# Optimization experiments

Measured on AMD Instinct MI355X. Metric: run time of the kernel, lower is better.

## Reference

```python
import jax, jax.numpy as jnp
import numpy as np

N_HEADS = 12
HIDDEN = 768  # NOTE: d_head == hidden_size in this module (unusual)

def setup_inputs() -> dict:
    key = jax.random.key(0)
    ks = jax.random.split(key, 4)
    b, s = 8, 512
    d3 = 3 * N_HEADS * HIDDEN
    return {
        "x": jax.random.normal(ks[0], (b, s, HIDDEN), dtype=jnp.float32),
        "mask": jnp.zeros((b, 1, 1, s), dtype=jnp.float32),
        "w_qkv": jax.random.normal(ks[1], (d3, HIDDEN), dtype=jnp.float32) * 0.02,
        "b_qkv": jnp.zeros((d3,), dtype=jnp.float32),
        "w_o": jax.random.normal(ks[2], (HIDDEN, N_HEADS * HIDDEN), dtype=jnp.float32) * 0.02,
        "b_o": jnp.zeros((HIDDEN,), dtype=jnp.float32),
    }

def reference(x, mask, w_qkv, b_qkv, w_o, b_o):
    b, s, _ = x.shape
    nh = N_HEADS * HIDDEN
    qkv = x @ w_qkv.T + b_qkv                      # (b, s, 3*n*h)
    q, k, v = jnp.split(qkv, 3, axis=-1)           # each (b, s, n*h)
    def heads(t):
        return t.reshape(b, s, N_HEADS, HIDDEN).transpose(0, 2, 1, 3)  # (b, n, s, h)
    q, k, v = heads(q), heads(k), heads(v)
    scale = 1.0 / np.sqrt(HIDDEN).astype(np.float32)
    scores = jnp.einsum('bnqh,bnkh->bnqk', q, k) * scale  # (b, n, s_q, s_k)
    scores = scores + mask                         # additive mask broadcast
    a = jax.nn.softmax(scores, axis=-1)
    av = jnp.einsum('bnqk,bnkh->bnqh', a, v)       # (b, n, s, h)
    h = av.transpose(0, 2, 1, 3).reshape(b, s, nh) # (b, s, n*h)
    return h @ w_o.T + b_o                         # (b, s, hidden)
```

## Files before the change

### kernel.cpp

```cpp
#include <hip/hip_runtime.h>
#include <hip/hip_bf16.h>
#include <stdint.h>

#define AS1 __attribute__((address_space(1)))
#define AS3 __attribute__((address_space(3)))

typedef __attribute__((ext_vector_type(8))) __bf16 bf16x8;
typedef __attribute__((ext_vector_type(4))) float f32x4;
typedef unsigned short u16;
typedef __attribute__((ext_vector_type(8))) unsigned short u16x8;

#define B_    8
#define S_    512
#define NH_   12
#define HD_   768
#define NHD_  (NH_*HD_)
#define D3_   (3*NHD_)
#define QKLD_ (2*NHD_)
#define QK_SCALE 0.03608439182435161f

__device__ __forceinline__ u16 f2bf(float x) {
  union { float f; unsigned u; } a; a.f = x;
  unsigned r = a.u + 0x7fffu + ((a.u >> 16) & 1u);
  return (u16)(r >> 16);
}
__device__ __forceinline__ float bf2f(u16 x) {
  union { unsigned u; float f; } a; a.u = ((unsigned)x) << 16; return a.f;
}

__device__ __forceinline__ void gload16(const void* g, void* l) {
  __builtin_amdgcn_global_load_lds((const AS1 void*)g, (AS3 void*)l, 16, 0, 0);
}

struct GP {
  const u16* A;
  const u16* B;
  int K, lda, ldb;
  long sAb, sAn, sBb, sBn;
  void* o0; void* o2;
  const float* bias;
};

template<int MODE>
__global__ __launch_bounds__(256)
void gemm_bt(GP p) {
  __shared__ __align__(16) char smem[32768];
  const int tid  = threadIdx.x;
  const int wave = tid >> 6, lane = tid & 63;
  const int wr = wave >> 1, wc = wave & 1;
  const int bm0 = blockIdx.y * 128;
  const int bn0 = blockIdx.x * 128;
  const int z   = blockIdx.z;
  const int zb  = z / NH_, zn = z - zb * NH_;

  const u16* A  = p.A + zb * p.sAb + zn * p.sAn;
  const u16* Bm = p.B + zb * p.sBb + zn * p.sBn;

  f32x4 acc[4][4];
  const f32x4 zero4 = {0.f, 0.f, 0.f, 0.f};
#pragma unroll
  for (int i = 0; i < 4; ++i)
#pragma unroll
    for (int j = 0; j < 4; ++j) acc[i][j] = zero4;

  const int scolsw = ((lane & 7) ^ (lane >> 3)) * 8;
  const u16* gA = A  + (size_t)(bm0 + wave*8 + (lane>>3)) * p.lda + scolsw;
  const u16* gB = Bm + (size_t)(bn0 + wave*8 + (lane>>3)) * p.ldb + scolsw;
  char* ldsA = smem;
  char* ldsB = smem + 16384;
  char* stA  = ldsA + wave*1024;
  char* stB  = ldsB + wave*1024;

  const int aRow = (wr*64 + (lane&15)) * 128;
  const int bRow = (wc*64 + (lane&15)) * 128;
  const int csw  = lane & 7;
  const int cOff0 = (((lane>>4)    ) ^ csw) << 4;
  const int cOff1 = ((4 + (lane>>4)) ^ csw) << 4;

  for (int k0 = 0; k0 < p.K; k0 += 64) {
#pragma unroll
    for (int i = 0; i < 4; ++i) {
      gload16(gA + (size_t)i*32*p.lda, stA + i*4096);
      gload16(gB + (size_t)i*32*p.ldb, stB + i*4096);
    }
    gA += 64; gB += 64;
    __syncthreads();
#pragma unroll
    for (int kk = 0; kk < 2; ++kk) {
      const int cOff = kk ? cOff1 : cOff0;
      bf16x8 av[4], bv[4];
#pragma unroll
      for (int i = 0; i < 4; ++i)
        av[i] = *(const bf16x8*)(ldsA + aRow + i*2048 + cOff);
#pragma unroll
      for (int j = 0; j < 4; ++j)
        bv[j] = *(const bf16x8*)(ldsB + bRow + j*2048 + cOff);
#pragma unroll
      for (int i = 0; i < 4; ++i)
#pragma unroll
        for (int j = 0; j < 4; ++j)
          acc[i][j] = __builtin_amdgcn_mfma_f32_16x16x32_bf16(av[i], bv[j], acc[i][j], 0, 0, 0);
    }
    __syncthreads();
  }

  const int r0 = bm0 + wr*64 + ((lane>>4) << 2);
  const int c0 = bn0 + wc*64 + (lane&15);

  if constexpr (MODE == 0) {
    if (bn0 < QKLD_) {
#pragma unroll
      for (int i = 0; i < 4; ++i) {
        u16* rbase = (u16*)p.o0 + (long)(r0 + i*16) * QKLD_;
#pragma unroll
        for (int j = 0; j < 4; ++j) {
          const int col = c0 + j*16;
          const float bs = p.bias[col];
#pragma unroll
          for (int r = 0; r < 4; ++r)
            rbase[(long)r * QKLD_ + col] = f2bf(acc[i][j][r] + bs);
        }
      }
    } else {
#pragma unroll
      for (int i = 0; i < 4; ++i) {
        const int rowq = r0 + i*16;
        const int s0 = rowq & 511;
        const int bb = rowq >> 9;
#pragma unroll
        for (int j = 0; j < 4; ++j) {
          const int col = c0 + j*16;
          const int vcol = col - QKLD_;
          const int n = vcol / HD_;
          const int h = vcol - n*HD_;
          const float bs = p.bias[col];
          ushort4 pk;
          pk.x = f2bf(acc[i][j][0] + bs);
          pk.y = f2bf(acc[i][j][1] + bs);
          pk.z = f2bf(acc[i][j][2] + bs);
          pk.w = f2bf(acc[i][j][3] + bs);
          *(ushort4*)((u16*)p.o2 + (long)(bb*NH_ + n)*(S_*HD_) + (long)h*S_ + s0) = pk;
        }
      }
    }
  } else {
#pragma unroll
    for (int i = 0; i < 4; ++i) {
#pragma unroll
      for (int j = 0; j < 4; ++j) {
        const int col = c0 + j*16;
#pragma unroll
        for (int r = 0; r < 4; ++r) {
          const int row = r0 + i*16 + r;
          const float v = acc[i][j][r];
          if constexpr (MODE == 1) {
            ((u16*)p.o0)[(long)z*S_*S_ + (long)row*S_ + col] = f2bf(v * QK_SCALE);
          } else if constexpr (MODE == 2) {
            ((u16*)p.o0)[(long)(zb*S_ + row)*QKLD_ + zn*HD_ + col] = f2bf(v);
          } else {
            ((float*)p.o0)[((long)z * gridDim.y * 128 + row) * HD_ + col] = v;
          }
        }
      }
    }
  }
}

__global__ __launch_bounds__(256)
void softmax_rows(u16* __restrict__ SP, const float* __restrict__ maskc) {
  const int wave = threadIdx.x >> 6, lane = threadIdx.x & 63;
  const int rid = blockIdx.x * 4 + wave;
  const int z = rid >> 9;
  const int b = z / NH_;
  const u16x8 sv = *(const u16x8*)(SP + (size_t)rid * S_ + lane*8);
  const float* mrow = maskc + (size_t)b * S_;
  float vals[8];
  float m = -3.4e38f;
#pragma unroll
  for (int j = 0; j < 8; ++j) {
    vals[j] = bf2f(sv[j]) + mrow[lane*8 + j];
    m = fmaxf(m, vals[j]);
  }
#pragma unroll
  for (int o = 32; o > 0; o >>= 1) m = fmaxf(m, __shfl_xor(m, o));
  float sum = 0.f;
#pragma unroll
  for (int j = 0; j < 8; ++j) { vals[j] = __expf(vals[j] - m); sum += vals[j]; }
#pragma unroll
  for (int o = 32; o > 0; o >>= 1) sum += __shfl_xor(sum, o);
  const float inv = 1.0f / sum;
  u16x8 pv;
#pragma unroll
  for (int j = 0; j < 8; ++j) pv[j] = f2bf(vals[j] * inv);
  *(u16x8*)(SP + (size_t)rid * S_ + lane*8) = pv;
}

__global__ __launch_bounds__(256)
void cvt_bf16(const float4* __restrict__ in, ushort4* __restrict__ out, int n4) {
  const int i = blockIdx.x * 256 + threadIdx.x;
  if (i >= n4) return;
  const float4 v = in[i];
  ushort4 o;
  o.x = f2bf(v.x); o.y = f2bf(v.y); o.z = f2bf(v.z); o.w = f2bf(v.w);
  out[i] = o;
}

__global__ __launch_bounds__(256)
void combine_out(const float4* __restrict__ part, const float* __restrict__ b,
                 float4* __restrict__ out, int n4) {
  const int i = blockIdx.x * 256 + threadIdx.x;
  if (i >= n4) return;
  const float4 a0 = part[i];
  const float4 a1 = part[i + (size_t)n4];
  const float4 a2 = part[i + (size_t)2*n4];
  const float4 a3 = part[i + (size_t)3*n4];
  const int c = (i * 4) % HD_;
  float4 o;
  o.x = a0.x + a1.x + a2.x + a3.x + b[c];
  o.y = a0.y + a1.y + a2.y + a3.y + b[c+1];
  o.z = a0.z + a1.z + a2.z + a3.z + b[c+2];
  o.w = a0.w + a1.w + a2.w + a3.w + b[c+3];
  out[i] = o;
}

extern "C" void kernel_launch(void* const* d_in, const int* in_sizes, int n_in,
                              void* d_out, int out_size, void* d_ws, size_t ws_size,
                              hipStream_t stream) {
  const float* x     = (const float*)d_in[0];
  const float* mask  = (const float*)d_in[1];
  const float* w_qkv = (const float*)d_in[2];
  const float* b_qkv = (const float*)d_in[3];
  const float* w_o   = (const float*)d_in[4];
  const float* b_o   = (const float*)d_in[5];
  float* out = (float*)d_out;

  int bc = 0;
  for (int c = 8; c >= 1; c >>= 1)
    if (56623104UL + (unsigned long)c*35389440UL <= ws_size) { bc = c; break; }
  if (bc == 0) return;

  char* ws = (char*)d_ws;
  u16* wqb = (u16*)(ws);
  u16* wob = (u16*)(ws + 42467328L);
  u16* xb  = (u16*)(ws + 56623104L);
  long off = 56623104L + (long)bc*786432L;
  u16* QKn = (u16*)(ws + off);  off += (long)bc*18874368L;
  u16* Vt  = (u16*)(ws + off);  off += (long)bc*9437184L;
  u16* SP  = (u16*)(ws + off);
  u16* H   = QKn;
  float* Part = (float*)SP;

  cvt_bf16<<<dim3(D3_*HD_/4/256), dim3(256), 0, stream>>>((const float4*)w_qkv, (ushort4*)wqb, D3_*HD_/4);
  cvt_bf16<<<dim3(HD_*NHD_/4/256), dim3(256), 0, stream>>>((const float4*)w_o, (ushort4*)wob, HD_*NHD_/4);

  const int nchunks = B_ / bc;
  const int rows_c = bc * S_;
  const int zc = bc * NH_;

  for (int c = 0; c < nchunks; ++c) {
    const long row0 = (long)c * rows_c;

    cvt_bf16<<<dim3(rows_c*HD_/4/256), dim3(256), 0, stream>>>(
        (const float4*)(x + row0*HD_), (ushort4*)xb, rows_c*HD_/4);

    GP p1; p1.A = xb; p1.B = wqb; p1.K = HD_; p1.lda = HD_; p1.ldb = HD_;
    p1.sAb = 0; p1.sAn = 0; p1.sBb = 0; p1.sBn = 0;
    p1.o0 = QKn; p1.o2 = Vt; p1.bias = b_qkv;
    gemm_bt<0><<<dim3(D3_/128, rows_c/128, 1), dim3(256), 0, stream>>>(p1);

    GP p2; p2.A = QKn; p2.B = QKn + NHD_; p2.K = HD_; p2.lda = QKLD_; p2.ldb = QKLD_;
    p2.sAb = (long)S_*QKLD_; p2.sAn = HD_;
    p2.sBb = (long)S_*QKLD_; p2.sBn = HD_;
    p2.o0 = SP; p2.o2 = nullptr; p2.bias = nullptr;
    gemm_bt<1><<<dim3(S_/128, S_/128, zc), dim3(256), 0, stream>>>(p2);

    softmax_rows<<<dim3(zc*S_/4), dim3(256), 0, stream>>>(SP, mask + (long)c*bc*S_);

    GP p3; p3.A = SP; p3.B = Vt; p3.K = S_; p3.lda = S_; p3.ldb = S_;
    p3.sAb = (long)NH_*S_*S_; p3.sAn = (long)S_*S_;
    p3.sBb = (long)NH_*S_*HD_; p3.sBn = (long)S_*HD_;
    p3.o0 = H; p3.o2 = nullptr; p3.bias = nullptr;
    gemm_bt<2><<<dim3(HD_/128, S_/128, zc), dim3(256), 0, stream>>>(p3);

    GP p4; p4.A = H; p4.B = wob; p4.K = NHD_/4; p4.lda = QKLD_; p4.ldb = NHD_;
    p4.sAb = 0; p4.sAn = NHD_/4;
    p4.sBb = 0; p4.sBn = NHD_/4;
    p4.o0 = Part; p4.o2 = nullptr; p4.bias = nullptr;
    gemm_bt<3><<<dim3(HD_/128, rows_c/128, 4), dim3(256), 0, stream>>>(p4);

    combine_out<<<dim3(rows_c*HD_/4/256), dim3(256), 0, stream>>>(
        (const float4*)Part, b_o, (float4*)(out + row0*HD_), rows_c*HD_/4);
  }
}
```

Measured before the change: 613.5 us.

## Remap GEMM blocks per XCD, template strides, and vectorize epilogue stores

```diff
diff --git a/kernel.cpp b/kernel.cpp
--- a/kernel.cpp
+++ b/kernel.cpp
@@ -27,6 +27,12 @@
 __device__ __forceinline__ float bf2f(u16 x) {
   union { unsigned u; float f; } a; a.u = ((unsigned)x) << 16; return a.f;
 }
+__device__ __forceinline__ uint2 pack4(float a, float b, float c, float d) {
+  uint2 r;
+  asm("v_cvt_pk_bf16_f32 %0, %1, %2" : "=v"(r.x) : "v"(a), "v"(b));
+  asm("v_cvt_pk_bf16_f32 %0, %1, %2" : "=v"(r.y) : "v"(c), "v"(d));
+  return r;
+}
 
 __device__ __forceinline__ void gload16(const void* g, void* l) {
   __builtin_amdgcn_global_load_lds((const AS1 void*)g, (AS3 void*)l, 16, 0, 0);
@@ -35,22 +41,41 @@
 struct GP {
   const u16* A;
   const u16* B;
-  int K, lda, ldb;
   long sAb, sAn, sBb, sBn;
   void* o0; void* o2;
   const float* bias;
+  int mMask, mShift, zPerX;
 };
 
-template<int MODE>
+template<int MODE, int LDA, int LDB, int KK>
 __global__ __launch_bounds__(256)
 void gemm_bt(GP p) {
   __shared__ __align__(16) char smem[32768];
   const int tid  = threadIdx.x;
   const int wave = tid >> 6, lane = tid & 63;
   const int wr = wave >> 1, wc = wave & 1;
-  const int bm0 = blockIdx.y * 128;
-  const int bn0 = blockIdx.x * 128;
-  const int z   = blockIdx.z;
+
+  const int bid = blockIdx.x;
+  const int xcd = bid & 7, loc = bid >> 3;
+  int m_idx, n_idx, z;
+  if constexpr (MODE == 0) {
+    m_idx = loc & p.mMask; n_idx = xcd * 27 + (loc >> p.mShift); z = 0;
+  } else if constexpr (MODE == 1) {
+    int inner;
+    if (p.zPerX) { inner = loc & 15; z = xcd * p.zPerX + (loc >> 4); }
+    else         { inner = bid & 15; z = bid >> 4; }
+    m_idx = inner >> 2; n_idx = inner & 3;
+  } else if constexpr (MODE == 2) {
+    int inner;
+    if (p.zPerX) { inner = loc % 24; z = xcd * p.zPerX + loc / 24; }
+    else         { inner = bid % 24; z = bid / 24; }
+    m_idx = inner / 6; n_idx = inner - (inner / 6) * 6;
+  } else {
+    m_idx = loc & p.mMask;
+    n_idx = (xcd & 1) * 3 + (loc >> p.mShift);
+    z = xcd >> 1;
+  }
+  const int bm0 = m_idx * 128, bn0 = n_idx * 128;
   const int zb  = z / NH_, zn = z - zb * NH_;
 
   const u16* A  = p.A + zb * p.sAb + zn * p.sAn;
@@ -64,8 +89,8 @@
     for (int j = 0; j < 4; ++j) acc[i][j] = zero4;
 
   const int scolsw = ((lane & 7) ^ (lane >> 3)) * 8;
-  const u16* gA = A  + (size_t)(bm0 + wave*8 + (lane>>3)) * p.lda + scolsw;
-  const u16* gB = Bm + (size_t)(bn0 + wave*8 + (lane>>3)) * p.ldb + scolsw;
+  const u16* gA = A  + (size_t)(bm0 + wave*8 + (lane>>3)) * LDA + scolsw;
+  const u16* gB = Bm + (size_t)(bn0 + wave*8 + (lane>>3)) * LDB + scolsw;
   char* ldsA = smem;
   char* ldsB = smem + 16384;
   char* stA  = ldsA + wave*1024;
@@ -77,11 +102,11 @@
   const int cOff0 = (((lane>>4)    ) ^ csw) << 4;
   const int cOff1 = ((4 + (lane>>4)) ^ csw) << 4;
 
-  for (int k0 = 0; k0 < p.K; k0 += 64) {
+  for (int k0 = 0; k0 < KK; k0 += 64) {
 #pragma unroll
     for (int i = 0; i < 4; ++i) {
-      gload16(gA + (size_t)i*32*p.lda, stA + i*4096);
-      gload16(gB + (size_t)i*32*p.ldb, stB + i*4096);
+      gload16(gA + (size_t)i*32*LDA, stA + i*4096);
+      gload16(gB + (size_t)i*32*LDB, stB + i*4096);
     }
     gA += 64; gB += 64;
     __syncthreads();
@@ -99,68 +124,46 @@
       for (int i = 0; i < 4; ++i)
 #pragma unroll
         for (int j = 0; j < 4; ++j)
-          acc[i][j] = __builtin_amdgcn_mfma_f32_16x16x32_bf16(av[i], bv[j], acc[i][j], 0, 0, 0);
+          acc[i][j] = __builtin_amdgcn_mfma_f32_16x16x32_bf16(bv[j], av[i], acc[i][j], 0, 0, 0);
     }
     __syncthreads();
   }
 
-  const int r0 = bm0 + wr*64 + ((lane>>4) << 2);
-  const int c0 = bn0 + wc*64 + (lane&15);
-
-  if constexpr (MODE == 0) {
-    if (bn0 < QKLD_) {
-#pragma unroll
-      for (int i = 0; i < 4; ++i) {
-        u16* rbase = (u16*)p.o0 + (long)(r0 + i*16) * QKLD_;
-#pragma unroll
-        for (int j = 0; j < 4; ++j) {
-          const int col = c0 + j*16;
-          const float bs = p.bias[col];
-#pragma unroll
-          for (int r = 0; r < 4; ++r)
-            rbase[(long)r * QKLD_ + col] = f2bf(acc[i][j][r] + bs);
+  const int mBase = bm0 + wr*64 + (lane & 15);
+  const int nBase = bn0 + wc*64 + ((lane >> 4) << 2);
+#pragma unroll
+  for (int i = 0; i < 4; ++i) {
+    const int m = mBase + i*16;
+#pragma unroll
+    for (int j = 0; j < 4; ++j) {
+      const int n = nBase + j*16;
+      const f32x4 v = acc[i][j];
+      if constexpr (MODE == 0) {
+        const float4 b4 = *(const float4*)(p.bias + n);
+        if (bn0 < QKLD_) {
+          *(uint2*)((u16*)p.o0 + (long)m * QKLD_ + n) =
+              pack4(v[0]+b4.x, v[1]+b4.y, v[2]+b4.z, v[3]+b4.w);
+        } else {
+          const int vcol = n - QKLD_;
+          const int nh = vcol / HD_;
+          const int h  = vcol - nh * HD_;
+          u16* vb = (u16*)p.o2 + (long)((m >> 9) * NH_ + nh) * (S_*HD_)
+                    + (long)h * S_ + (m & 511);
+          vb[0]    = f2bf(v[0]+b4.x);
+          vb[512]  = f2bf(v[1]+b4.y);
+          vb[1024] = f2bf(v[2]+b4.z);
+          vb[1536] = f2bf(v[3]+b4.w);
         }
-      }
-    } else {
-#pragma unroll
-      for (int i = 0; i < 4; ++i) {
-        const int rowq = r0 + i*16;
-        const int s0 = rowq & 511;
-        const int bb = rowq >> 9;
-#pragma unroll
-        for (int j = 0; j < 4; ++j) {
-          const int col = c0 + j*16;
-          const int vcol = col - QKLD_;
-          const int n = vcol / HD_;
-          const int h = vcol - n*HD_;
-          const float bs = p.bias[col];
-          ushort4 pk;
-          pk.x = f2bf(acc[i][j][0] + bs);
-          pk.y = f2bf(acc[i][j][1] + bs);
-          pk.z = f2bf(acc[i][j][2] + bs);
-          pk.w = f2bf(acc[i][j][3] + bs);
-          *(ushort4*)((u16*)p.o2 + (long)(bb*NH_ + n)*(S_*HD_) + (long)h*S_ + s0) = pk;
-        }
-      }
-    }
-  } else {
-#pragma unroll
-    for (int i = 0; i < 4; ++i) {
-#pragma unroll
-      for (int j = 0; j < 4; ++j) {
-        const int col = c0 + j*16;
-#pragma unroll
-        for (int r = 0; r < 4; ++r) {
-          const int row = r0 + i*16 + r;
-          const float v = acc[i][j][r];
-          if constexpr (MODE == 1) {
-            ((u16*)p.o0)[(long)z*S_*S_ + (long)row*S_ + col] = f2bf(v * QK_SCALE);
-          } else if constexpr (MODE == 2) {
-            ((u16*)p.o0)[(long)(zb*S_ + row)*QKLD_ + zn*HD_ + col] = f2bf(v);
-          } else {
-            ((float*)p.o0)[((long)z * gridDim.y * 128 + row) * HD_ + col] = v;
-          }
-        }
+      } else if constexpr (MODE == 1) {
+        *(uint2*)((u16*)p.o0 + (long)z*S_*S_ + (long)m*S_ + n) =
+            pack4(v[0]*QK_SCALE, v[1]*QK_SCALE, v[2]*QK_SCALE, v[3]*QK_SCALE);
+      } else if constexpr (MODE == 2) {
+        *(uint2*)((u16*)p.o0 + (long)(zb*S_ + m)*QKLD_ + zn*HD_ + n) =
+            pack4(v[0], v[1], v[2], v[3]);
+      } else {
+        const long rowsTot = (long)(p.mMask + 1) * 128;
+        *(float4*)((float*)p.o0 + ((long)z * rowsTot + m) * HD_ + n) =
+            *(const float4*)&v;
       }
     }
   }
@@ -256,6 +259,9 @@
   const int nchunks = B_ / bc;
   const int rows_c = bc * S_;
   const int zc = bc * NH_;
+  const int mT = rows_c / 128;
+  const int mShift = __builtin_ctz(mT);
+  const int zPerX = (zc % 8 == 0) ? zc / 8 : 0;
 
   for (int c = 0; c < nchunks; ++c) {
     const long row0 = (long)c * rows_c;
@@ -263,30 +269,34 @@
     cvt_bf16<<<dim3(rows_c*HD_/4/256), dim3(256), 0, stream>>>(
         (const float4*)(x + row0*HD_), (ushort4*)xb, rows_c*HD_/4);
 
-    GP p1; p1.A = xb; p1.B = wqb; p1.K = HD_; p1.lda = HD_; p1.ldb = HD_;
+    GP p1; p1.A = xb; p1.B = wqb;
     p1.sAb = 0; p1.sAn = 0; p1.sBb = 0; p1.sBn = 0;
     p1.o0 = QKn; p1.o2 = Vt; p1.bias = b_qkv;
-    gemm_bt<0><<<dim3(D3_/128, rows_c/128, 1), dim3(256), 0, stream>>>(p1);
-
-    GP p2; p2.A = QKn; p2.B = QKn + NHD_; p2.K = HD_; p2.lda = QKLD_; p2.ldb = QKLD_;
+    p1.mMask = mT - 1; p1.mShift = mShift; p1.zPerX = 0;
+    gemm_bt<0, HD_, HD_, HD_><<<dim3(216 * mT), dim3(256), 0, stream>>>(p1);
+
+    GP p2; p2.A = QKn; p2.B = QKn + NHD_;
     p2.sAb = (long)S_*QKLD_; p2.sAn = HD_;
     p2.sBb = (long)S_*QKLD_; p2.sBn = HD_;
     p2.o0 = SP; p2.o2 = nullptr; p2.bias = nullptr;
-    gemm_bt<1><<<dim3(S_/128, S_/128, zc), dim3(256), 0, stream>>>(p2);
+    p2.mMask = 0; p2.mShift = 0; p2.zPerX = zPerX;
+    gemm_bt<1, QKLD_, QKLD_, HD_><<<dim3(zc * 16), dim3(256), 0, stream>>>(p2);
 
     softmax_rows<<<dim3(zc*S_/4), dim3(256), 0, stream>>>(SP, mask + (long)c*bc*S_);
 
-    GP p3; p3.A = SP; p3.B = Vt; p3.K = S_; p3.lda = S_; p3.ldb = S_;
+    GP p3; p3.A = SP; p3.B = Vt;
     p3.sAb = (long)NH_*S_*S_; p3.sAn = (long)S_*S_;
     p3.sBb = (long)NH_*S_*HD_; p3.sBn = (long)S_*HD_;
     p3.o0 = H; p3.o2 = nullptr; p3.bias = nullptr;
-    gemm_bt<2><<<dim3(HD_/128, S_/128, zc), dim3(256), 0, stream>>>(p3);
-
-    GP p4; p4.A = H; p4.B = wob; p4.K = NHD_/4; p4.lda = QKLD_; p4.ldb = NHD_;
+    p3.mMask = 0; p3.mShift = 0; p3.zPerX = zPerX;
+    gemm_bt<2, S_, S_, S_><<<dim3(zc * 24), dim3(256), 0, stream>>>(p3);
+
+    GP p4; p4.A = H; p4.B = wob;
     p4.sAb = 0; p4.sAn = NHD_/4;
     p4.sBb = 0; p4.sBn = NHD_/4;
     p4.o0 = Part; p4.o2 = nullptr; p4.bias = nullptr;
-    gemm_bt<3><<<dim3(HD_/128, rows_c/128, 4), dim3(256), 0, stream>>>(p4);
+    p4.mMask = mT - 1; p4.mShift = mShift; p4.zPerX = 0;
+    gemm_bt<3, QKLD_, NHD_, NHD_/4><<<dim3(24 * mT), dim3(256), 0, stream>>>(p4);
 
     combine_out<<<dim3(rows_c*HD_/4/256), dim3(256), 0, stream>>>(
         (const float4*)Part, b_o, (float4*)(out + row0*HD_), rows_c*HD_/4);
```

Result: no change. 611.3 us (-0.3%).
